# Performance work log

Hardware: AMD Instinct MI355X
Metric: run time of the kernel (lower is better)

Reference implementation:

```python
import jax, jax.numpy as jnp
import numpy as np

COMMITMENT_COST = 0.25


def setup_inputs() -> dict:
    key = jax.random.key(0)
    k1, k2 = jax.random.split(key, 2)
    inputs = jax.random.normal(k1, (8, 2048, 1024), dtype=jnp.float32)
    # per-head codebooks: [H=4, K=1024, dh=256]
    codebook = jax.random.normal(k2, (4, 1024, 256), dtype=jnp.float32)
    return {"inputs": inputs, "codebook": codebook}


def reference(inputs, codebook):
    H, K, dh = codebook.shape
    flat = inputs.reshape(-1, H, dh)  # [N, H, dh]
    # squared-euclidean distances per head: [H, N, K]
    x_sq = jnp.sum(flat * flat, axis=-1).T[:, :, None]          # [H, N, 1]
    c_sq = jnp.sum(codebook * codebook, axis=-1)[:, None, :]    # [H, 1, K]
    dots = jnp.einsum('nhd,hkd->hnk', flat, codebook)           # [H, N, K]
    distances = x_sq + c_sq - 2.0 * dots
    idx = jnp.argmin(distances, axis=-1)                        # [H, N]
    # gather codebook rows (equivalent to one-hot @ codebook)
    q = jnp.take_along_axis(codebook, idx[:, :, None], axis=1)  # [H, N, dh]
    quantized = jnp.transpose(q, (1, 0, 2)).reshape(inputs.shape)
    # ema=True, eval mode: q_latent_loss = 0
    e_latent_loss = jnp.mean((jax.lax.stop_gradient(quantized) - inputs) ** 2)
    loss = COMMITMENT_COST * e_latent_loss
    # residual=False: straight-through estimator
    quantized_out = inputs + jax.lax.stop_gradient(quantized - inputs)
    return loss, quantized_out
```

## Files before the change

kernel.cpp:

```cpp
#include <hip/hip_runtime.h>
#include <cfloat>

#define NH    4
#define NK    1024
#define DHD   256
#define NTOK  16384
#define ROWS  (NH * DHD)

typedef __attribute__((ext_vector_type(8))) short bf16x8;
typedef __attribute__((ext_vector_type(4))) float f32x4;

#define WS_CSQ  ((size_t)0)
#define WS_BH   ((size_t)16384)
#define WS_BL   (WS_BH + (size_t)2097152)
#define WS_CAND (WS_BL + (size_t)2097152)
#define WS_NEED (WS_CAND + (size_t)524288)

__device__ __forceinline__ unsigned short f32_to_bf16_rn(float f) {
    unsigned u = __float_as_uint(f);
    u += 0x7FFFu + ((u >> 16) & 1u);
    return (unsigned short)(u >> 16);
}
__device__ __forceinline__ float bf16_as_f32(unsigned short h) {
    return __uint_as_float(((unsigned)h) << 16);
}

__device__ __forceinline__ void gload_lds16(const uint4* g, uint4* l) {
    __builtin_amdgcn_global_load_lds(
        (const __attribute__((address_space(1))) void*)g,
        (__attribute__((address_space(3))) void*)l, 16, 0, 0);
}

__global__ __launch_bounds__(64) void csq_kernel(const float* __restrict__ cb,
                                                 float* __restrict__ csq) {
    const int code = blockIdx.x;
    const int lane = threadIdx.x;
    const float4 v = *(const float4*)(cb + (size_t)code * DHD + lane * 4);
    float s = v.x * v.x + v.y * v.y + v.z * v.z + v.w * v.w;
#pragma unroll
    for (int off = 32; off > 0; off >>= 1) s += __shfl_down(s, off, 64);
    if (lane == 0) csq[code] = s;
}

__global__ __launch_bounds__(256) void cvt_cb_kernel(const float* __restrict__ cb,
                                                     uint4* __restrict__ bch,
                                                     uint4* __restrict__ bcl,
                                                     float* __restrict__ csq) {
    const int g = blockIdx.x * 8 + (threadIdx.x >> 5);
    const int o = threadIdx.x & 31;
    const float* src = cb + (size_t)g * DHD + o * 8;
    unsigned wh[4], wl[4];
    float s = 0.f;
#pragma unroll
    for (int i = 0; i < 4; ++i) {
        const float f0 = src[2 * i], f1 = src[2 * i + 1];
        s += f0 * f0 + f1 * f1;
        const unsigned short h0 = f32_to_bf16_rn(f0);
        const unsigned short h1 = f32_to_bf16_rn(f1);
        const unsigned short l0 = f32_to_bf16_rn(f0 - bf16_as_f32(h0));
        const unsigned short l1 = f32_to_bf16_rn(f1 - bf16_as_f32(h1));
        wh[i] = (unsigned)h0 | ((unsigned)h1 << 16);
        wl[i] = (unsigned)l0 | ((unsigned)l1 << 16);
    }
    const int hh = g >> 10, c = g & 1023, dc = o >> 2, kk = o & 3;
    const size_t unit = (size_t)((hh * 8 + dc) * 4 + kk) * NK + c;
    bch[unit] = make_uint4(wh[0], wh[1], wh[2], wh[3]);
    bcl[unit] = make_uint4(wl[0], wl[1], wl[2], wl[3]);
#pragma unroll
    for (int m = 16; m > 0; m >>= 1) s += __shfl_xor(s, m, 32);
    if (o == 0) csq[g] = s;
}

__device__ __forceinline__ bool lt_vi(float v, int i, float w, int j) {
    return (v < w) || (v == w && i < j);
}

__device__ __forceinline__ float np_sq_pairwise256(const float* __restrict__ a) {
#pragma clang fp contract(off)
    float tot = 0.f;
#pragma unroll
    for (int blk = 0; blk < 2; ++blk) {
        const float* p = a + blk * 128;
        float r0 = p[0] * p[0], r1 = p[1] * p[1], r2 = p[2] * p[2], r3 = p[3] * p[3];
        float r4 = p[4] * p[4], r5 = p[5] * p[5], r6 = p[6] * p[6], r7 = p[7] * p[7];
#pragma clang loop unroll_count(2)
        for (int i = 8; i < 128; i += 8) {
            r0 = r0 + p[i + 0] * p[i + 0];
            r1 = r1 + p[i + 1] * p[i + 1];
            r2 = r2 + p[i + 2] * p[i + 2];
            r3 = r3 + p[i + 3] * p[i + 3];
            r4 = r4 + p[i + 4] * p[i + 4];
            r5 = r5 + p[i + 5] * p[i + 5];
            r6 = r6 + p[i + 6] * p[i + 6];
            r7 = r7 + p[i + 7] * p[i + 7];
        }
        const float res = ((r0 + r1) + (r2 + r3)) + ((r4 + r5) + (r6 + r7));
        tot = (blk == 0) ? res : (tot + res);
    }
    return tot;
}

__device__ __forceinline__ float np_dot_seq256(const float* __restrict__ a,
                                               const float* __restrict__ b) {
#pragma clang fp contract(off)
    float s = 0.f;
#pragma clang loop unroll_count(4)
    for (int i = 0; i < 256; ++i) s = s + a[i] * b[i];
    return s;
}

__device__ __forceinline__ void refine_exact(const float* __restrict__ xr,
                                             const float* __restrict__ cr,
                                             float& Xo, float& Co, float& Do) {
#pragma clang fp contract(off)
    float s = 0.f;
    float X = 0.f, C = 0.f;
    for (int blk = 0; blk < 2; ++blk) {
        const float4* xq = (const float4*)(xr + blk * 128);
        const float4* cq = (const float4*)(cr + blk * 128);
        float xa[8], ca[8];
#pragma unroll
        for (int j = 0; j < 8; ++j) { xa[j] = 0.f; ca[j] = 0.f; }
#pragma clang loop unroll_count(4)
        for (int g = 0; g < 16; ++g) {
            const float4 a0 = xq[2 * g], a1 = xq[2 * g + 1];
            const float4 b0 = cq[2 * g], b1 = cq[2 * g + 1];
            const float xf[8] = {a0.x, a0.y, a0.z, a0.w, a1.x, a1.y, a1.z, a1.w};
            const float cf[8] = {b0.x, b0.y, b0.z, b0.w, b1.x, b1.y, b1.z, b1.w};
#pragma unroll
            for (int j = 0; j < 8; ++j) {
                xa[j] = xa[j] + xf[j] * xf[j];
                ca[j] = ca[j] + cf[j] * cf[j];
            }
#pragma unroll
            for (int j = 0; j < 8; ++j) s = s + xf[j] * cf[j];
        }
        const float xres = ((xa[0] + xa[1]) + (xa[2] + xa[3])) + ((xa[4] + xa[5]) + (xa[6] + xa[7]));
        const float cres = ((ca[0] + ca[1]) + (ca[2] + ca[3])) + ((ca[4] + ca[5]) + (ca[6] + ca[7]));
        X = (blk == 0) ? xres : (X + xres);
        C = (blk == 0) ? cres : (C + cres);
    }
    Xo = X; Co = C; Do = s;
}

#define BT 64
#define KT 32
#define NTIL (NK / KT)

__global__ __launch_bounds__(256, 2) void vq_mfma(const float* __restrict__ x,
                                                  const float* __restrict__ csq,
                                                  const uint4* __restrict__ bch,
                                                  const uint4* __restrict__ bcl,
                                                  int* __restrict__ candw) {
    __shared__ uint4 BsH[1024];
    __shared__ uint4 BsL[1024];
    __shared__ float Cs[NK];

    const int tid  = threadIdx.x;
    const int h    = blockIdx.y;
    const int t0   = blockIdx.x * BT;
    const int wv   = tid >> 6;
    const int lane = tid & 63;
    const int kk   = lane >> 4;
    const int ln   = lane & 15;

#pragma unroll
    for (int i = tid; i < NK; i += 256) Cs[i] = csq[h * NK + i];

    bf16x8 aH[8], aL[8];
    {
        const int tokb = t0 + wv * 16 + ln;
        const float* xa = x + (size_t)tokb * ROWS + h * DHD + kk * 8;
#pragma unroll
        for (int dc = 0; dc < 8; ++dc) {
            const float* p = xa + dc * 32;
            const float4 f0 = *(const float4*)p;
            const float4 f1 = *(const float4*)(p + 4);
            const float f[8] = {f0.x, f0.y, f0.z, f0.w, f1.x, f1.y, f1.z, f1.w};
            bf16x8 hv, lv;
#pragma unroll
            for (int j = 0; j < 8; ++j) {
                const unsigned short hb = f32_to_bf16_rn(f[j]);
                hv[j] = (short)hb;
                lv[j] = (short)f32_to_bf16_rn(f[j] - bf16_as_f32(hb));
            }
            aH[dc] = hv;
            aL[dc] = lv;
        }
    }

    float b1[4], b2[4];
    int   i1[4], i2[4];
#pragma unroll
    for (int s = 0; s < 4; ++s) { b1[s] = FLT_MAX; b2[s] = FLT_MAX; i1[s] = 0; i2[s] = 0; }

    for (int t = 0; t < NTIL; ++t) {
        const int k0 = t * KT;
        __syncthreads();
#pragma unroll
        for (int p = 0; p < 4; ++p) {
            const int q   = wv * 4 + p;
            const int row = 2 * q + (lane >> 5);
            const size_t w = (size_t)(h * 32 + row) * NK + k0 + (lane & 31);
            gload_lds16(&bch[w], &BsH[q * 64]);
            gload_lds16(&bcl[w], &BsL[q * 64]);
        }
        __syncthreads();

        f32x4 acc[2];
#pragma unroll
        for (int ct = 0; ct < 2; ++ct) acc[ct] = (f32x4){0.f, 0.f, 0.f, 0.f};

#pragma unroll
        for (int dc = 0; dc < 8; ++dc) {
#pragma unroll
            for (int ct = 0; ct < 2; ++ct) {
                const int bu = (dc * 4 + kk) * 32 + ct * 16 + ln;
                const bf16x8 bH = *(const bf16x8*)&BsH[bu];
                const bf16x8 bL = *(const bf16x8*)&BsL[bu];
                acc[ct] = __builtin_amdgcn_mfma_f32_16x16x32_bf16(aH[dc], bH, acc[ct], 0, 0, 0);
                acc[ct] = __builtin_amdgcn_mfma_f32_16x16x32_bf16(aH[dc], bL, acc[ct], 0, 0, 0);
                acc[ct] = __builtin_amdgcn_mfma_f32_16x16x32_bf16(aL[dc], bH, acc[ct], 0, 0, 0);
            }
        }

#pragma unroll
        for (int ct = 0; ct < 2; ++ct) {
            const float cs   = Cs[k0 + ct * 16 + ln];
            const int   codg = k0 + ct * 16 + ln;
#pragma unroll
            for (int r = 0; r < 4; ++r) {
                const float dist = cs - 2.f * acc[ct][r];
                if (dist < b1[r]) { b2[r] = b1[r]; i2[r] = i1[r]; b1[r] = dist; i1[r] = codg; }
                else if (dist < b2[r]) { b2[r] = dist; i2[r] = codg; }
            }
        }
    }

#pragma unroll
    for (int s = 0; s < 4; ++s) {
        float v1 = b1[s], v2 = b2[s];
        int   j1 = i1[s], j2 = i2[s];
#pragma unroll
        for (int m = 1; m <= 8; m <<= 1) {
            const float o1 = __shfl_xor(v1, m, 64);
            const int   oj1 = __shfl_xor(j1, m, 64);
            const float o2 = __shfl_xor(v2, m, 64);
            const int   oj2 = __shfl_xor(j2, m, 64);
            if (lt_vi(o1, oj1, v1, j1)) {
                if (lt_vi(v1, j1, o2, oj2)) { v2 = v1; j2 = j1; }
                else                        { v2 = o2; j2 = oj2; }
                v1 = o1; j1 = oj1;
            } else if (lt_vi(o1, oj1, v2, j2)) {
                v2 = o1; j2 = oj1;
            }
        }
        if (ln == 0) {
            const int tl  = wv * 16 + kk * 4 + s;
            const int gid = h * NTOK + t0 + tl;
            candw[2 * gid + 0] = j1;
            candw[2 * gid + 1] = j2;
        }
    }
}

__global__ __launch_bounds__(64) void vq_tail(const float* __restrict__ x,
                                              const float* __restrict__ cb,
                                              const int* __restrict__ candw,
                                              float* __restrict__ out) {
    const int lane = threadIdx.x;
    const int rowb = blockIdx.x * 32;
    const int h    = rowb >> 14;
    const int tb   = rowb & (NTOK - 1);
    const float* cbh = cb + (size_t)h * NK * DHD;

    const int rloc = lane >> 1;
    const int cand = lane & 1;
    const int row  = rowb + rloc;
    const int t    = tb + rloc;
    const int code = candw[2 * row + cand];
    const float* xr = x + (size_t)t * ROWS + h * DHD;
    const float* cr = cbh + (size_t)code * DHD;
    float X, C, D;
    refine_exact(xr, cr, X, C, D);
    float d;
    {
#pragma clang fp contract(off)
        const float tt = X + C;
        d = tt - 2.0f * D;
    }
    const float od = __shfl_xor(d, 1, 64);
    int   sel  = code;
    float lacc = 0.f;
    if (cand == 0) {
        const int jB = candw[2 * row + 1];
        const bool pickB = (od < d) || (od == d && jB < code);
        sel  = pickB ? jB : code;
        lacc = pickB ? od : d;
    }

    for (int r = 0; r < 32; ++r) {
        const int cr_code = __shfl(sel, 2 * r, 64);
        const int tr = tb + r;
        const float4 q4 = *(const float4*)(cbh + (size_t)cr_code * DHD + (lane << 2));
        *(float4*)(out + 1 + (size_t)tr * ROWS + h * DHD + (lane << 2)) = q4;
    }
#pragma unroll
    for (int off = 32; off > 0; off >>= 1) lacc += __shfl_down(lacc, off, 64);
    if (lane == 0) atomicAdd(out, lacc * (0.25f / 16777216.f));
}

#define TN 128
#define TK 128
#define KC 16
#define APAD 4
#define BPAD 4

__global__ __launch_bounds__(256, 2) void vq_main_fp32(const float* __restrict__ x,
                                                       const float* __restrict__ cb,
                                                       const float* __restrict__ csq,
                                                       float* __restrict__ out) {
    __shared__ float As[KC][TN + APAD];
    __shared__ float Bs[KC][TK + BPAD];
    __shared__ float Cs[TK];
    __shared__ int   Cand[TN][2];
    __shared__ int   SIdx[TN];
    __shared__ float WSum[4];

    const int tid = threadIdx.x;
    const int h   = blockIdx.y;
    const int t0  = blockIdx.x * TN;
    const int ty  = tid >> 4;
    const int tx  = tid & 15;

    const float* xh  = x  + (size_t)t0 * ROWS + h * DHD;
    const float* cbh = cb + (size_t)h * NK * DHD;

    const int sr = tid >> 1;
    const int sd = (tid & 1) << 3;

    float b1[8], b2[8];
    int   i1[8], i2[8];
#pragma unroll
    for (int r = 0; r < 8; ++r) { b1[r] = FLT_MAX; b2[r] = FLT_MAX; i1[r] = 0; i2[r] = 0; }

    for (int k0 = 0; k0 < NK; k0 += TK) {
        __syncthreads();
        if (tid < TK) Cs[tid] = csq[h * NK + k0 + tid];

        float acc[8][8];
#pragma unroll
        for (int r = 0; r < 8; ++r)
#pragma unroll
            for (int c = 0; c < 8; ++c) acc[r][c] = 0.f;

        for (int d0 = 0; d0 < DHD; d0 += KC) {
            __syncthreads();
            {
                const float* ap = xh + (size_t)sr * ROWS + d0 + sd;
                const float4 a0 = *(const float4*)ap;
                const float4 a1 = *(const float4*)(ap + 4);
                As[sd + 0][sr] = a0.x; As[sd + 1][sr] = a0.y;
                As[sd + 2][sr] = a0.z; As[sd + 3][sr] = a0.w;
                As[sd + 4][sr] = a1.x; As[sd + 5][sr] = a1.y;
                As[sd + 6][sr] = a1.z; As[sd + 7][sr] = a1.w;
            }
            {
                const float* bp = cbh + (size_t)(k0 + sr) * DHD + d0 + sd;
                const float4 b0v = *(const float4*)bp;
                const float4 b1v = *(const float4*)(bp + 4);
                Bs[sd + 0][sr] = b0v.x; Bs[sd + 1][sr] = b0v.y;
                Bs[sd + 2][sr] = b0v.z; Bs[sd + 3][sr] = b0v.w;
                Bs[sd + 4][sr] = b1v.x; Bs[sd + 5][sr] = b1v.y;
                Bs[sd + 6][sr] = b1v.z; Bs[sd + 7][sr] = b1v.w;
            }
            __syncthreads();
#pragma unroll 4
            for (int kc = 0; kc < KC; ++kc) {
                const float4 a0 = *(const float4*)&As[kc][ty << 3];
                const float4 a1 = *(const float4*)&As[kc][(ty << 3) + 4];
                const float4 p0 = *(const float4*)&Bs[kc][tx << 2];
                const float4 p1 = *(const float4*)&Bs[kc][64 + (tx << 2)];
                const float aa[8] = {a0.x, a0.y, a0.z, a0.w, a1.x, a1.y, a1.z, a1.w};
                const float bb[8] = {p0.x, p0.y, p0.z, p0.w, p1.x, p1.y, p1.z, p1.w};
#pragma unroll
                for (int r = 0; r < 8; ++r)
#pragma unroll
                    for (int c = 0; c < 8; ++c)
                        acc[r][c] = fmaf(aa[r], bb[c], acc[r][c]);
            }
        }
#pragma unroll
        for (int r = 0; r < 8; ++r) {
#pragma unroll
            for (int c = 0; c < 8; ++c) {
                const int cc = (c < 4) ? ((tx << 2) + c) : (64 + (tx << 2) + c - 4);
                const float dist = Cs[cc] - 2.f * acc[r][c];
                const int   idx  = k0 + cc;
                if (dist < b1[r]) { b2[r] = b1[r]; i2[r] = i1[r]; b1[r] = dist; i1[r] = idx; }
                else if (dist < b2[r]) { b2[r] = dist; i2[r] = idx; }
            }
        }
    }

#pragma unroll
    for (int r = 0; r < 8; ++r) {
        float v1 = b1[r], v2 = b2[r];
        int   j1 = i1[r], j2 = i2[r];
#pragma unroll
        for (int m = 1; m <= 8; m <<= 1) {
            const float o1 = __shfl_xor(v1, m, 64);
            const int   oj1 = __shfl_xor(j1, m, 64);
            const float o2 = __shfl_xor(v2, m, 64);
            const int   oj2 = __shfl_xor(j2, m, 64);
            if (lt_vi(o1, oj1, v1, j1)) {
                if (lt_vi(v1, j1, o2, oj2)) { v2 = v1; j2 = j1; }
                else                        { v2 = o2; j2 = oj2; }
                v1 = o1; j1 = oj1;
            } else if (lt_vi(o1, oj1, v2, j2)) {
                v2 = o1; j2 = oj1;
            }
        }
        b1[r] = v1; i1[r] = j1; b2[r] = v2; i2[r] = j2;
    }
    if (tx == 0) {
#pragma unroll
        for (int r = 0; r < 8; ++r) {
            Cand[(ty << 3) + r][0] = i1[r];
            Cand[(ty << 3) + r][1] = i2[r];
        }
    }
    __syncthreads();

    {
        const int token = tid >> 1;
        const int cand  = tid & 1;
        const int code  = Cand[token][cand];
        const float* xr = xh + (size_t)token * ROWS;
        const float* cr = cbh + (size_t)code * DHD;
        const float X = np_sq_pairwise256(xr);
        const float C = np_sq_pairwise256(cr);
        const float D = np_dot_seq256(xr, cr);
        float d;
        {
#pragma clang fp contract(off)
            const float t = X + C;
            d = t - 2.0f * D;
        }
        const float od = __shfl_xor(d, 1, 64);
        if (cand == 0) {
            const int jA = code;
            const int jB = Cand[token][1];
            const bool pickB = (od < d) || (od == d && jB < jA);
            SIdx[token] = pickB ? jB : jA;
        }
    }
    __syncthreads();

    const int wav  = tid >> 6;
    const int lane = tid & 63;
    float lacc = 0.f;
    for (int t = wav; t < TN; t += 4) {
        const float4 q4 = *(const float4*)(cbh + (size_t)SIdx[t] * DHD + (lane << 2));
        const float4 x4 = *(const float4*)(xh + (size_t)t * ROWS + (lane << 2));
        const float dx = q4.x - x4.x, dy = q4.y - x4.y;
        const float dz = q4.z - x4.z, dw = q4.w - x4.w;
        lacc += dx * dx + dy * dy + dz * dz + dw * dw;
        *(float4*)(out + 1 + (size_t)(t0 + t) * ROWS + h * DHD + (lane << 2)) = q4;
    }
#pragma unroll
    for (int off = 32; off > 0; off >>= 1) lacc += __shfl_down(lacc, off, 64);
    if (lane == 0) WSum[wav] = lacc;
    __syncthreads();
    if (tid == 0) {
        const float s = WSum[0] + WSum[1] + WSum[2] + WSum[3];
        atomicAdd(out, s * (0.25f / 16777216.f));
    }
}

extern "C" void kernel_launch(void* const* d_in, const int* in_sizes, int n_in,
                              void* d_out, int out_size, void* d_ws, size_t ws_size,
                              hipStream_t stream) {
    const float* x   = (const float*)d_in[0];
    const float* cb  = (const float*)d_in[1];
    float*       out = (float*)d_out;
    char*        ws  = (char*)d_ws;
    float*       csq = (float*)(ws + WS_CSQ);

    hipMemsetAsync(d_out, 0, sizeof(float), stream);

    if (ws_size >= WS_NEED) {
        uint4* bch   = (uint4*)(ws + WS_BH);
        uint4* bcl   = (uint4*)(ws + WS_BL);
        int*   candw = (int*)(ws + WS_CAND);
        cvt_cb_kernel<<<NH * NK / 8, 256, 0, stream>>>(cb, bch, bcl, csq);
        dim3 grid(NTOK / BT, NH);
        vq_mfma<<<grid, 256, 0, stream>>>(x, csq, bch, bcl, candw);
        vq_tail<<<NTOK * NH / 32, 64, 0, stream>>>(x, cb, candw, out);
    } else {
        csq_kernel<<<NH * NK, 64, 0, stream>>>(cb, csq);
        dim3 grid(NTOK / TN, NH);
        vq_main_fp32<<<grid, 256, 0, stream>>>(x, cb, csq, out);
    }
}
```

Measured before the change: 286.6 us.

## Double-buffer codebook tiles in LDS and halve the code tile width

Splits the shared codebook buffers into two halves and prefetches the next tile of codebook codes while computing MFMAs on the current one, going from two barriers per tile to one. To fit the same LDS footprint the code tile shrinks from 32 to 16 codes, so there are twice as many iterations and barriers. The aim is to hide global-to-LDS load latency behind compute. The cost is less MFMA work per tile and a single accumulator chain, which may expose MFMA dependency latency.

New measurement: 330.8 us. +15.4%, slower.

```diff
diff --git a/kernel.cpp b/kernel.cpp
--- a/kernel.cpp
+++ b/kernel.cpp
@@ -144,16 +144,28 @@
 }
 
 #define BT 64
-#define KT 32
+#define KT 16
 #define NTIL (NK / KT)
+
+#define STAGE_TILE(BUF, K0)                                                      \
+    {                                                                            \
+        _Pragma("unroll")                                                        \
+        for (int p_ = 0; p_ < 2; ++p_) {                                         \
+            const int q_   = wv * 2 + p_;                                        \
+            const int row_ = q_ * 4 + (lane >> 4);                               \
+            const size_t w_ = (size_t)(h * 32 + row_) * NK + (K0) + (lane & 15); \
+            gload_lds16(&bch[w_], &BsH[BUF][q_ * 64]);                           \
+            gload_lds16(&bcl[w_], &BsL[BUF][q_ * 64]);                           \
+        }                                                                        \
+    }
 
 __global__ __launch_bounds__(256, 2) void vq_mfma(const float* __restrict__ x,
                                                   const float* __restrict__ csq,
                                                   const uint4* __restrict__ bch,
                                                   const uint4* __restrict__ bcl,
                                                   int* __restrict__ candw) {
-    __shared__ uint4 BsH[1024];
-    __shared__ uint4 BsL[1024];
+    __shared__ uint4 BsH[2][512];
+    __shared__ uint4 BsL[2][512];
     __shared__ float Cs[NK];
 
     const int tid  = threadIdx.x;
@@ -164,6 +176,8 @@
     const int kk   = lane >> 4;
     const int ln   = lane & 15;
 
+    STAGE_TILE(0, 0)
+
 #pragma unroll
     for (int i = tid; i < NK; i += 256) Cs[i] = csq[h * NK + i];
 
@@ -194,47 +208,37 @@
 #pragma unroll
     for (int s = 0; s < 4; ++s) { b1[s] = FLT_MAX; b2[s] = FLT_MAX; i1[s] = 0; i2[s] = 0; }
 
+    __syncthreads();
+    int cur = 0;
+
     for (int t = 0; t < NTIL; ++t) {
         const int k0 = t * KT;
-        __syncthreads();
-#pragma unroll
-        for (int p = 0; p < 4; ++p) {
-            const int q   = wv * 4 + p;
-            const int row = 2 * q + (lane >> 5);
-            const size_t w = (size_t)(h * 32 + row) * NK + k0 + (lane & 31);
-            gload_lds16(&bch[w], &BsH[q * 64]);
-            gload_lds16(&bcl[w], &BsL[q * 64]);
-        }
-        __syncthreads();
-
-        f32x4 acc[2];
-#pragma unroll
-        for (int ct = 0; ct < 2; ++ct) acc[ct] = (f32x4){0.f, 0.f, 0.f, 0.f};
-
+        if (t + 1 < NTIL) STAGE_TILE(cur ^ 1, k0 + KT)
+
+        f32x4 acc = (f32x4){0.f, 0.f, 0.f, 0.f};
 #pragma unroll
         for (int dc = 0; dc < 8; ++dc) {
-#pragma unroll
-            for (int ct = 0; ct < 2; ++ct) {
-                const int bu = (dc * 4 + kk) * 32 + ct * 16 + ln;
-                const bf16x8 bH = *(const bf16x8*)&BsH[bu];
-                const bf16x8 bL = *(const bf16x8*)&BsL[bu];
-                acc[ct] = __builtin_amdgcn_mfma_f32_16x16x32_bf16(aH[dc], bH, acc[ct], 0, 0, 0);
-                acc[ct] = __builtin_amdgcn_mfma_f32_16x16x32_bf16(aH[dc], bL, acc[ct], 0, 0, 0);
-                acc[ct] = __builtin_amdgcn_mfma_f32_16x16x32_bf16(aL[dc], bH, acc[ct], 0, 0, 0);
-            }
-        }
-
-#pragma unroll
-        for (int ct = 0; ct < 2; ++ct) {
-            const float cs   = Cs[k0 + ct * 16 + ln];
-            const int   codg = k0 + ct * 16 + ln;
+            const int bu = (dc * 4 + kk) * 16 + ln;
+            const bf16x8 bH = *(const bf16x8*)&BsH[cur][bu];
+            const bf16x8 bL = *(const bf16x8*)&BsL[cur][bu];
+            acc = __builtin_amdgcn_mfma_f32_16x16x32_bf16(aH[dc], bH, acc, 0, 0, 0);
+            acc = __builtin_amdgcn_mfma_f32_16x16x32_bf16(aH[dc], bL, acc, 0, 0, 0);
+            acc = __builtin_amdgcn_mfma_f32_16x16x32_bf16(aL[dc], bH, acc, 0, 0, 0);
+        }
+
+        {
+            const float cs   = Cs[k0 + ln];
+            const int   codg = k0 + ln;
 #pragma unroll
             for (int r = 0; r < 4; ++r) {
-                const float dist = cs - 2.f * acc[ct][r];
+                const float dist = cs - 2.f * acc[r];
                 if (dist < b1[r]) { b2[r] = b1[r]; i2[r] = i1[r]; b1[r] = dist; i1[r] = codg; }
                 else if (dist < b2[r]) { b2[r] = dist; i2[r] = codg; }
             }
         }
+
+        __syncthreads();
+        cur ^= 1;
     }
 
 #pragma unroll
```
